# Kernel optimization log

Hardware: AMD Instinct MI355X
Metric: run time of the kernel (lower is better)

The kernel has to match this reference:

```python
import jax, jax.numpy as jnp
import numpy as np

N = 50000      # nodes
E = 800000     # edges (before self loops)
F_IN = 512     # input feature dim (num_features)
D = 128        # hidden_dim
NBLK = 3       # num_layers - 1
EPS = 1e-5


def _layernorm(x, g, b):
    mu = x.mean(-1, keepdims=True)
    var = ((x - mu) ** 2).mean(-1, keepdims=True)
    return (x - mu) / jnp.sqrt(var + EPS) * g + b


def _gatv2(x, Wl, bl, Wr, br, att, bias, src, dst, n):
    # PyG GATv2Conv, heads=1, eval mode (attention dropout off), self loops in src/dst
    xl = x @ Wl + bl                      # [N, D] messages (x_j side)
    xr = x @ Wr + br                      # [N, D] target side (x_i)
    e = jax.nn.leaky_relu(xl[src] + xr[dst], negative_slope=0.2)  # [E', D]
    score = e @ att                       # [E']
    smax = jax.ops.segment_max(score, dst, num_segments=n)
    ex = jnp.exp(score - smax[dst])
    denom = jax.ops.segment_sum(ex, dst, num_segments=n)
    alpha = ex / denom[dst]               # segment softmax over incoming edges
    out = jax.ops.segment_sum(alpha[:, None] * xl[src], dst, num_segments=n)
    return out + bias


def setup_inputs() -> dict:
    key = jax.random.key(0)
    ks = jax.random.split(key, 32)
    w = lambda k, shape: (jax.random.normal(k, shape, jnp.float32) * 0.02)
    p = {}
    p["x"] = jax.random.normal(ks[0], (N, F_IN), jnp.float32)
    p["edge_index"] = jax.random.randint(ks[1], (2, E), 0, N)
    p["emb_W"] = w(ks[2], (F_IN, D)); p["emb_b"] = jnp.zeros((D,), jnp.float32)
    p["ln1_g"] = jnp.ones((NBLK, D), jnp.float32); p["ln1_b"] = jnp.zeros((NBLK, D), jnp.float32)
    p["gat_Wl"] = w(ks[3], (NBLK, D, D)); p["gat_bl"] = jnp.zeros((NBLK, D), jnp.float32)
    p["gat_Wr"] = w(ks[4], (NBLK, D, D)); p["gat_br"] = jnp.zeros((NBLK, D), jnp.float32)
    p["gat_att"] = w(ks[5], (NBLK, D)); p["gat_bias"] = jnp.zeros((NBLK, D), jnp.float32)
    for i in range(NBLK):
        h = D * (i + 1)  # mlp_ratio = level = i+1
        p[f"mlp_w1_{i}"] = w(ks[6 + 2 * i], (D, h))
        p[f"mlp_w2_{i}"] = w(ks[7 + 2 * i], (h, D))
    p["attn_Wa"] = w(ks[12], (D, D)); p["attn_ba"] = jnp.zeros((D,), jnp.float32)
    p["attn_Wb"] = w(ks[13], (D, D)); p["attn_bb"] = jnp.zeros((D,), jnp.float32)
    p["attn_Wc"] = w(ks[14], (D, 1)); p["attn_bc"] = jnp.zeros((1,), jnp.float32)
    p["rho_W"] = w(ks[15], (D, D)); p["rho_b"] = jnp.zeros((D,), jnp.float32)
    p["cls_W"] = w(ks[16], (D, 4)); p["cls_b"] = jnp.zeros((4,), jnp.float32)
    return p


def reference(x, edge_index, emb_W, emb_b, ln1_g, ln1_b, gat_Wl, gat_bl, gat_Wr, gat_br,
              gat_att, gat_bias, mlp_w1_0, mlp_w2_0, mlp_w1_1, mlp_w2_1, mlp_w1_2, mlp_w2_2,
              attn_Wa, attn_ba, attn_Wb, attn_bb, attn_Wc, attn_bc, rho_W, rho_b, cls_W, cls_b):
    n = x.shape[0]
    sl = jnp.arange(n, dtype=edge_index.dtype)
    src = jnp.concatenate([edge_index[0], sl])  # add self loops (GATv2Conv default)
    dst = jnp.concatenate([edge_index[1], sl])
    h = jax.nn.relu(x @ emb_W + emb_b)          # embedding (dropout off)
    mlps = [(mlp_w1_0, mlp_w2_0), (mlp_w1_1, mlp_w2_1), (mlp_w1_2, mlp_w2_2)]
    for i in range(NBLK):
        hn = _layernorm(h, ln1_g[i], ln1_b[i])
        h = h + _gatv2(hn, gat_Wl[i], gat_bl[i], gat_Wr[i], gat_br[i], gat_att[i], gat_bias[i], src, dst, n)
        w1, w2 = mlps[i]
        # NOTE: original forward applies channel_mix directly on x (norm2 is unused)
        h = h + jax.nn.gelu(h @ w1, approximate=False) @ w2
    # Attn_Net_Gated pooling
    a = jnp.tanh(h @ attn_Wa + attn_ba)
    b = jax.nn.sigmoid(h @ attn_Wb + attn_bb)
    A = ((a * b) @ attn_Wc + attn_bc).T          # [1, N]
    h_path = jax.nn.softmax(A, axis=1) @ h       # [1, D]
    hr = jax.nn.relu(h_path @ rho_W + rho_b)
    logits = hr @ cls_W + cls_b                  # [1, 4]
    Y_hat = jnp.argmax(logits, axis=1, keepdims=True)
    hazards = jax.nn.sigmoid(logits)
    S = jnp.cumprod(1.0 - hazards, axis=1)
    return (hazards, S, Y_hat, logits)
```

## Files before the change

### kernel.cpp

```cpp
#include <hip/hip_runtime.h>
#include <math.h>


#define D 128
#define NBLK 3
#define STG_STRIDE 132
#define S16 136
#define ROWS 128
#define BT 512

typedef __attribute__((ext_vector_type(8))) short bf16x8;
typedef __attribute__((ext_vector_type(4))) float f32x4;

static __device__ __forceinline__ float bf2f(unsigned short u) {
    union { unsigned i; float f; } c; c.i = ((unsigned)u) << 16; return c.f;
}
static __device__ __forceinline__ unsigned short f2bf(float f) {
    union { float f; unsigned i; } c; c.f = f;
    unsigned r = c.i + 0x7fff + ((c.i >> 16) & 1);
    return (unsigned short)(r >> 16);
}
static __device__ __forceinline__ void gl16(const unsigned short* g, unsigned short* l) {
    __builtin_amdgcn_global_load_lds((const __attribute__((address_space(1))) void*)g,
                                     (__attribute__((address_space(3))) void*)l, 16, 0, 0);
}
static __device__ __forceinline__ float gelu_f(float x) {
    return 0.5f * x * (1.f + erff(x * 0.70710678118654752f));
}

__global__ void zero_k(int* deg, int* fill, float* red, int n) {
    int i = blockIdx.x * blockDim.x + threadIdx.x;
    if (i < n) { deg[i] = 0; fill[i] = 0; }
    if (i < 132) red[i] = 0.f;
}

__global__ void hist_k(const int* __restrict__ dst, int* __restrict__ deg, int E) {
    int e = blockIdx.x * blockDim.x + threadIdx.x;
    if (e < E) atomicAdd(&deg[dst[e]], 1);
}

__global__ __launch_bounds__(256) void blockscan_k(const int* __restrict__ deg,
                                                   int* __restrict__ rowptr,
                                                   int* __restrict__ bsum, int n) {
    __shared__ int tmp[256];
    const int tid = threadIdx.x;
    const int i = blockIdx.x * 256 + tid;
    int v = (i < n) ? deg[i] : 0;
    tmp[tid] = v;
    __syncthreads();
#pragma unroll
    for (int off = 1; off < 256; off <<= 1) {
        int t = (tid >= off) ? tmp[tid - off] : 0;
        __syncthreads();
        tmp[tid] += t;
        __syncthreads();
    }
    if (i < n) rowptr[i + 1] = tmp[tid];
    if (tid == 255) bsum[blockIdx.x] = tmp[255];
}

__global__ __launch_bounds__(256) void scansums_k(int* __restrict__ bsum, int nb) {
    __shared__ int tmp[256];
    const int tid = threadIdx.x;
    int v = (tid < nb) ? bsum[tid] : 0;
    tmp[tid] = v;
    __syncthreads();
#pragma unroll
    for (int off = 1; off < 256; off <<= 1) {
        int t = (tid >= off) ? tmp[tid - off] : 0;
        __syncthreads();
        tmp[tid] += t;
        __syncthreads();
    }
    if (tid < nb) bsum[tid] = tmp[tid];
}

__global__ __launch_bounds__(256) void addoff_k(int* __restrict__ rowptr,
                                                const int* __restrict__ bsum, int n) {
    int i = blockIdx.x * 256 + threadIdx.x;
    if (i == 0) rowptr[0] = 0;
    if (i < n && blockIdx.x > 0) rowptr[i + 1] += bsum[blockIdx.x - 1];
}

__global__ void scatter_k(const int* __restrict__ src, const int* __restrict__ dst,
                          const int* __restrict__ rowptr, int* __restrict__ fill,
                          int* __restrict__ esrc, int E) {
    int e = blockIdx.x * blockDim.x + threadIdx.x;
    if (e < E) {
        int d = dst[e];
        int pos = rowptr[d] + atomicAdd(&fill[d], 1);
        esrc[pos] = src[e];
    }
}

struct WDesc { const float* s; unsigned short* d; int K; int M; };
struct WPack { WDesc w[21]; };

__global__ __launch_bounds__(256) void wprep_k(WPack p) {
    WDesc d = p.w[blockIdx.y];
    const int nc = d.K / 32;
    const int chunks = (d.M / 16) * nc * 64;
    for (int i = blockIdx.x * 256 + threadIdx.x; i < chunks; i += gridDim.x * 256) {
        const int l = i & 63;
        const int c = (i >> 6) % nc;
        const int t = i / (64 * nc);
        const int m = t * 16 + (l & 15);
        const int kb = c * 32 + ((l >> 4) & 3) * 8;
#pragma unroll
        for (int j = 0; j < 8; ++j)
            d.d[(size_t)i * 8 + j] = f2bf(d.s[(size_t)(kb + j) * d.M + m]);
    }
}

__global__ __launch_bounds__(256) void bcat_k(const float* bl, const float* br,
                                              const float* ba, const float* bb,
                                              float* sb) {
    const int t = threadIdx.x;
    for (int i = 0; i < 3; ++i)
        sb[i * 256 + t] = (t < 128) ? bl[i * 128 + t] : br[i * 128 + t - 128];
    sb[3 * 256 + t] = (t < 128) ? ba[t] : bb[t - 128];
}


static __device__ __forceinline__ void stage_blob(const unsigned short* src,
                                                  unsigned short* wls, int tid) {
#pragma unroll
    for (int i = 0; i < 4; ++i) {
        const int idx = i * BT + tid;
        gl16(src + (size_t)idx * 8, &wls[idx * 8]);
    }
}

static __device__ __forceinline__ void pf_issue(const unsigned short* src, int tid,
                                                float4 pf[4]) {
#pragma unroll
    for (int i = 0; i < 4; ++i)
        pf[i] = *(const float4*)(src + (size_t)(i * BT + tid) * 8);
}
static __device__ __forceinline__ void pf_commit(unsigned short* wls, int tid,
                                                 const float4 pf[4]) {
#pragma unroll
    for (int i = 0; i < 4; ++i)
        *(float4*)(&wls[(i * BT + tid) * 8]) = pf[i];
}

static __device__ __forceinline__ void mfma32(const bf16x8 a[4],
                                              const unsigned short* wls,
                                              int l, f32x4 acc[8]) {
#pragma unroll
    for (int c = 0; c < 4; ++c)
#pragma unroll
        for (int t = 0; t < 8; ++t) {
            const bf16x8 bfr = *(const bf16x8*)&wls[((t * 4 + c) * 64 + l) * 8];
            acc[t] = __builtin_amdgcn_mfma_f32_16x16x32_bf16(a[c], bfr, acc[t], 0, 0, 0);
        }
}

static __device__ __forceinline__ void ln_row(float av[4][8], const float* lng,
                                              const float* lnb, int q) {
    float s = 0.f;
#pragma unroll
    for (int c = 0; c < 4; ++c)
#pragma unroll
        for (int j = 0; j < 8; ++j) s += av[c][j];
    s += __shfl_xor(s, 16, 64); s += __shfl_xor(s, 32, 64);
    const float mu = s * (1.f / 128.f);
    float vv = 0.f;
#pragma unroll
    for (int c = 0; c < 4; ++c)
#pragma unroll
        for (int j = 0; j < 8; ++j) { const float dd = av[c][j] - mu; vv += dd * dd; }
    vv += __shfl_xor(vv, 16, 64); vv += __shfl_xor(vv, 32, 64);
    const float rs = rsqrtf(vv * (1.f / 128.f) + 1e-5f);
#pragma unroll
    for (int c = 0; c < 4; ++c) {
        const int kb = c * 32 + q * 8;
        const float4 g0 = *(const float4*)(lng + kb);
        const float4 g1 = *(const float4*)(lng + kb + 4);
        const float4 b0 = *(const float4*)(lnb + kb);
        const float4 b1 = *(const float4*)(lnb + kb + 4);
        const float gg[8] = {g0.x, g0.y, g0.z, g0.w, g1.x, g1.y, g1.z, g1.w};
        const float bb[8] = {b0.x, b0.y, b0.z, b0.w, b1.x, b1.y, b1.z, b1.w};
#pragma unroll
        for (int j = 0; j < 8; ++j)
            av[c][j] = (av[c][j] - mu) * rs * gg[j] + bb[j];
    }
}

static __device__ __forceinline__ void xwrite(const f32x4 acc[8], const float* sb256,
                                              unsigned short* X, int rnd, int rowbase,
                                              int w, int q, int l15, int N) {
#pragma unroll
    for (int t = 0; t < 8; ++t) {
        const int col = rnd * 128 + t * 16 + l15;
        const float bv = sb256[col];
#pragma unroll
        for (int rr = 0; rr < 4; ++rr) {
            const int row = rowbase + w * 16 + q * 4 + rr;
            if (row < N) X[(size_t)row * 256 + col] = f2bf(acc[t][rr] + bv);
        }
    }
}

__global__ __launch_bounds__(BT) void start_k(const float* __restrict__ x,
                                              const unsigned short* __restrict__ embc,
                                              const float* __restrict__ emb_b,
                                              const unsigned short* __restrict__ gatc,
                                              const float* __restrict__ lng,
                                              const float* __restrict__ lnb,
                                              const float* __restrict__ sb256,
                                              float* __restrict__ H,
                                              unsigned short* __restrict__ X, int N) {
    __shared__ __align__(16) char smem[ROWS * STG_STRIDE * 4];
    unsigned short* wls = (unsigned short*)smem;
    float* stg = (float*)smem;
    const int tid = threadIdx.x;
    const int w = tid >> 6, l = tid & 63, q = l >> 4, l15 = l & 15;
    const int rowbase = blockIdx.x * ROWS;
    int r = rowbase + w * 16 + l15;
    const bool rv = r < N; if (!rv) r = N - 1;
    float4 pf[4];

    f32x4 accH[8];
#pragma unroll
    for (int t = 0; t < 8; ++t) accH[t] = (f32x4){0.f, 0.f, 0.f, 0.f};

    stage_blob(embc, wls, tid);
    __syncthreads();

#pragma unroll
    for (int rnd = 0; rnd < 4; ++rnd) {
        const unsigned short* nb = (rnd < 3) ? embc + (size_t)(rnd + 1) * 16384 : gatc;
        pf_issue(nb, tid, pf);
        bf16x8 afr[4];
#pragma unroll
        for (int c = 0; c < 4; ++c) {
            const float* ap = x + (size_t)r * 512 + rnd * 128 + c * 32 + q * 8;
            const float4 v0 = *(const float4*)ap;
            const float4 v1 = *(const float4*)(ap + 4);
            afr[c][0] = (short)f2bf(v0.x); afr[c][1] = (short)f2bf(v0.y);
            afr[c][2] = (short)f2bf(v0.z); afr[c][3] = (short)f2bf(v0.w);
            afr[c][4] = (short)f2bf(v1.x); afr[c][5] = (short)f2bf(v1.y);
            afr[c][6] = (short)f2bf(v1.z); afr[c][7] = (short)f2bf(v1.w);
        }
        mfma32(afr, wls, l, accH);
        __syncthreads();
        if (rnd < 3) { pf_commit(wls, tid, pf); __syncthreads(); }
    }

#pragma unroll
    for (int t = 0; t < 8; ++t) {
        const int col = t * 16 + l15;
        const float bv = emb_b[col];
#pragma unroll
        for (int rr = 0; rr < 4; ++rr) {
            const int row = rowbase + w * 16 + q * 4 + rr;
            const float hv = fmaxf(accH[t][rr] + bv, 0.f);
            if (row < N) H[(size_t)row * D + col] = hv;
            stg[(w * 16 + q * 4 + rr) * STG_STRIDE + col] = hv;
        }
    }
    float av[4][8];
#pragma unroll
    for (int c = 0; c < 4; ++c)
#pragma unroll
        for (int j = 0; j < 8; ++j)
            av[c][j] = stg[(w * 16 + l15) * STG_STRIDE + c * 32 + q * 8 + j];
    ln_row(av, lng, lnb, q);
    bf16x8 xfr[4];
#pragma unroll
    for (int c = 0; c < 4; ++c)
#pragma unroll
        for (int j = 0; j < 8; ++j) xfr[c][j] = (short)f2bf(av[c][j]);

    __syncthreads();
    pf_commit(wls, tid, pf);
    __syncthreads();

    pf_issue(gatc + 16384, tid, pf);
    f32x4 acc[8];
#pragma unroll
    for (int t = 0; t < 8; ++t) acc[t] = (f32x4){0.f, 0.f, 0.f, 0.f};
    mfma32(xfr, wls, l, acc);
    xwrite(acc, sb256, X, 0, rowbase, w, q, l15, N);
    __syncthreads();
    pf_commit(wls, tid, pf);
    __syncthreads();

#pragma unroll
    for (int t = 0; t < 8; ++t) acc[t] = (f32x4){0.f, 0.f, 0.f, 0.f};
    mfma32(xfr, wls, l, acc);
    xwrite(acc, sb256, X, 1, rowbase, w, q, l15, N);
}

template <int NMR>
__global__ __launch_bounds__(BT) void bridge_k(float* __restrict__ H,
                                               const unsigned short* __restrict__ w1c,
                                               const unsigned short* __restrict__ w2c,
                                               const unsigned short* __restrict__ gatc,
                                               const float* __restrict__ lng,
                                               const float* __restrict__ lnb,
                                               const float* __restrict__ sb256,
                                               unsigned short* __restrict__ X, int N) {
    __shared__ __align__(16) char smem[ROWS * STG_STRIDE * 4];
    unsigned short* wls   = (unsigned short*)smem;
    unsigned short* stg16 = (unsigned short*)(smem + 32768);
    float*          stgF  = (float*)smem;
    const int tid = threadIdx.x;
    const int w = tid >> 6, l = tid & 63, q = l >> 4, l15 = l & 15;
    const int rowbase = blockIdx.x * ROWS;
    int r = rowbase + w * 16 + l15;
    const bool rv = r < N; if (!rv) r = N - 1;
    float4 pf[4];

    stage_blob(w1c, wls, tid);

    float av[4][8];
    bf16x8 afr[4];
#pragma unroll
    for (int c = 0; c < 4; ++c) {
        const float* ap = H + (size_t)r * D + c * 32 + q * 8;
        const float4 v0 = *(const float4*)ap;
        const float4 v1 = *(const float4*)(ap + 4);
        av[c][0] = v0.x; av[c][1] = v0.y; av[c][2] = v0.z; av[c][3] = v0.w;
        av[c][4] = v1.x; av[c][5] = v1.y; av[c][6] = v1.z; av[c][7] = v1.w;
#pragma unroll
        for (int j = 0; j < 8; ++j) afr[c][j] = (short)f2bf(av[c][j]);
    }

    f32x4 accH[8];
#pragma unroll
    for (int t = 0; t < 8; ++t) accH[t] = (f32x4){0.f, 0.f, 0.f, 0.f};
    __syncthreads();

#pragma unroll
    for (int rnd = 0; rnd < NMR; ++rnd) {
        pf_issue(w2c + (size_t)rnd * 16384, tid, pf);
        f32x4 accT[8];
#pragma unroll
        for (int t = 0; t < 8; ++t) accT[t] = (f32x4){0.f, 0.f, 0.f, 0.f};
        mfma32(afr, wls, l, accT);
#pragma unroll
        for (int t = 0; t < 8; ++t)
#pragma unroll
            for (int rr = 0; rr < 4; ++rr)
                stg16[(w * 16 + q * 4 + rr) * S16 + t * 16 + l15] = f2bf(gelu_f(accT[t][rr]));
        __syncthreads();
        pf_commit(wls, tid, pf);
        __syncthreads();
        const unsigned short* nb = (rnd + 1 < NMR) ? w1c + (size_t)(rnd + 1) * 16384 : gatc;
        pf_issue(nb, tid, pf);
        bf16x8 tfr[4];
#pragma unroll
        for (int c = 0; c < 4; ++c)
            tfr[c] = *(const bf16x8*)&stg16[(w * 16 + l15) * S16 + c * 32 + q * 8];
        mfma32(tfr, wls, l, accH);
        __syncthreads();
        if (rnd + 1 < NMR) { pf_commit(wls, tid, pf); __syncthreads(); }
    }

#pragma unroll
    for (int t = 0; t < 8; ++t)
#pragma unroll
        for (int rr = 0; rr < 4; ++rr)
            stgF[(w * 16 + q * 4 + rr) * STG_STRIDE + t * 16 + l15] = accH[t][rr];
#pragma unroll
    for (int c = 0; c < 4; ++c)
#pragma unroll
        for (int j = 0; j < 8; ++j)
            av[c][j] += stgF[(w * 16 + l15) * STG_STRIDE + c * 32 + q * 8 + j];

    if (rv) {
#pragma unroll
        for (int c = 0; c < 4; ++c) {
            float* hp = H + (size_t)r * D + c * 32 + q * 8;
            *(float4*)hp       = make_float4(av[c][0], av[c][1], av[c][2], av[c][3]);
            *(float4*)(hp + 4) = make_float4(av[c][4], av[c][5], av[c][6], av[c][7]);
        }
    }

    ln_row(av, lng, lnb, q);
    bf16x8 xfr[4];
#pragma unroll
    for (int c = 0; c < 4; ++c)
#pragma unroll
        for (int j = 0; j < 8; ++j) xfr[c][j] = (short)f2bf(av[c][j]);

    __syncthreads();
    pf_commit(wls, tid, pf);
    __syncthreads();

    pf_issue(gatc + 16384, tid, pf);
    f32x4 acc[8];
#pragma unroll
    for (int t = 0; t < 8; ++t) acc[t] = (f32x4){0.f, 0.f, 0.f, 0.f};
    mfma32(xfr, wls, l, acc);
    xwrite(acc, sb256, X, 0, rowbase, w, q, l15, N);
    __syncthreads();
    pf_commit(wls, tid, pf);
    __syncthreads();

#pragma unroll
    for (int t = 0; t < 8; ++t) acc[t] = (f32x4){0.f, 0.f, 0.f, 0.f};
    mfma32(xfr, wls, l, acc);
    xwrite(acc, sb256, X, 1, rowbase, w, q, l15, N);
}

__global__ __launch_bounds__(BT) void head_k(const float* __restrict__ H,
                                             const unsigned short* __restrict__ w1c,
                                             const unsigned short* __restrict__ w2c,
                                             const unsigned short* __restrict__ attc,
                                             const float* __restrict__ sb256,
                                             const float* __restrict__ Wc,
                                             const float* __restrict__ bc,
                                             float* __restrict__ red, int N) {
    __shared__ __align__(16) char smem[ROWS * STG_STRIDE * 4];
    unsigned short* wls   = (unsigned short*)smem;
    unsigned short* stg16 = (unsigned short*)(smem + 32768);
    float*          stgF  = (float*)smem;
    __shared__ float sacc[8][128];
    __shared__ float sdn[8];
    const int tid = threadIdx.x;
    const int w = tid >> 6, l = tid & 63, q = l >> 4, l15 = l & 15;
    const int rowbase = blockIdx.x * ROWS;
    int r = rowbase + w * 16 + l15;
    if (r > N - 1) r = N - 1;
    float4 pf[4];

    stage_blob(w1c, wls, tid);

    float av[4][8];
    bf16x8 afr[4];
#pragma unroll
    for (int c = 0; c < 4; ++c) {
        const float* ap = H + (size_t)r * D + c * 32 + q * 8;
        const float4 v0 = *(const float4*)ap;
        const float4 v1 = *(const float4*)(ap + 4);
        av[c][0] = v0.x; av[c][1] = v0.y; av[c][2] = v0.z; av[c][3] = v0.w;
        av[c][4] = v1.x; av[c][5] = v1.y; av[c][6] = v1.z; av[c][7] = v1.w;
#pragma unroll
        for (int j = 0; j < 8; ++j) afr[c][j] = (short)f2bf(av[c][j]);
    }

    f32x4 accH[8];
#pragma unroll
    for (int t = 0; t < 8; ++t) accH[t] = (f32x4){0.f, 0.f, 0.f, 0.f};
    __syncthreads();

#pragma unroll
    for (int rnd = 0; rnd < 3; ++rnd) {
        pf_issue(w2c + (size_t)rnd * 16384, tid, pf);
        f32x4 accT[8];
#pragma unroll
        for (int t = 0; t < 8; ++t) accT[t] = (f32x4){0.f, 0.f, 0.f, 0.f};
        mfma32(afr, wls, l, accT);
#pragma unroll
        for (int t = 0; t < 8; ++t)
#pragma unroll
            for (int rr = 0; rr < 4; ++rr)
                stg16[(w * 16 + q * 4 + rr) * S16 + t * 16 + l15] = f2bf(gelu_f(accT[t][rr]));
        __syncthreads();
        pf_commit(wls, tid, pf);
        __syncthreads();
        const unsigned short* nb = (rnd + 1 < 3) ? w1c + (size_t)(rnd + 1) * 16384 : attc;
        pf_issue(nb, tid, pf);
        bf16x8 tfr[4];
#pragma unroll
        for (int c = 0; c < 4; ++c)
            tfr[c] = *(const bf16x8*)&stg16[(w * 16 + l15) * S16 + c * 32 + q * 8];
        mfma32(tfr, wls, l, accH);
        __syncthreads();
        if (rnd + 1 < 3) { pf_commit(wls, tid, pf); __syncthreads(); }
    }

#pragma unroll
    for (int t = 0; t < 8; ++t)
#pragma unroll
        for (int rr = 0; rr < 4; ++rr)
            stgF[(w * 16 + q * 4 + rr) * STG_STRIDE + t * 16 + l15] = accH[t][rr];
#pragma unroll
    for (int c = 0; c < 4; ++c)
#pragma unroll
        for (int j = 0; j < 8; ++j)
            av[c][j] += stgF[(w * 16 + l15) * STG_STRIDE + c * 32 + q * 8 + j];
#pragma unroll
    for (int c = 0; c < 4; ++c)
#pragma unroll
        for (int j = 0; j < 8; ++j) afr[c][j] = (short)f2bf(av[c][j]);

    __syncthreads();
    pf_commit(wls, tid, pf);
    __syncthreads();

    pf_issue(attc + 16384, tid, pf);
    float th[8][4];
    f32x4 acc[8];
#pragma unroll
    for (int t = 0; t < 8; ++t) acc[t] = (f32x4){0.f, 0.f, 0.f, 0.f};
    mfma32(afr, wls, l, acc);
#pragma unroll
    for (int t = 0; t < 8; ++t) {
        const float bv = sb256[t * 16 + l15];
#pragma unroll
        for (int rr = 0; rr < 4; ++rr) th[t][rr] = tanhf(acc[t][rr] + bv);
    }
    __syncthreads();
    pf_commit(wls, tid, pf);
    __syncthreads();

#pragma unroll
    for (int t = 0; t < 8; ++t) acc[t] = (f32x4){0.f, 0.f, 0.f, 0.f};
    mfma32(afr, wls, l, acc);

    float pa[4] = {0.f, 0.f, 0.f, 0.f};
#pragma unroll
    for (int t = 0; t < 8; ++t) {
        const float bv = sb256[128 + t * 16 + l15];
        const float wcv = Wc[t * 16 + l15];
#pragma unroll
        for (int rr = 0; rr < 4; ++rr) {
            const float sg = 1.f / (1.f + __expf(-(acc[t][rr] + bv)));
            pa[rr] = fmaf(th[t][rr] * sg, wcv, pa[rr]);
        }
    }
#pragma unroll
    for (int m = 1; m < 16; m <<= 1)
#pragma unroll
        for (int rr = 0; rr < 4; ++rr) pa[rr] += __shfl_xor(pa[rr], m, 64);

    const float bcv = bc[0];
    float wgt[4];
#pragma unroll
    for (int rr = 0; rr < 4; ++rr) {
        const int row = rowbase + w * 16 + q * 4 + rr;
        wgt[rr] = (row < N) ? __expf(pa[rr] + bcv) : 0.f;
    }
    float s = wgt[0] + wgt[1] + wgt[2] + wgt[3];
    s += __shfl_xor(s, 16, 64);
    s += __shfl_xor(s, 32, 64);
    if (l == 0) sdn[w] = s;

    const int sl = ((l15 >> 2) << 4);
    float wv[4];
#pragma unroll
    for (int rr = 0; rr < 4; ++rr) wv[rr] = __shfl(wgt[rr], sl, 64);
    const int rsel = l15 & 3;
    const float wm = (rsel == 0) ? wv[0] : (rsel == 1) ? wv[1] : (rsel == 2) ? wv[2] : wv[3];

#pragma unroll
    for (int c = 0; c < 4; ++c) {
        float pv[8];
#pragma unroll
        for (int j = 0; j < 8; ++j) pv[j] = wm * av[c][j];
#pragma unroll
        for (int m = 1; m < 16; m <<= 1)
#pragma unroll
            for (int j = 0; j < 8; ++j) pv[j] += __shfl_xor(pv[j], m, 64);
        if (l15 == 0) {
#pragma unroll
            for (int j = 0; j < 8; ++j) sacc[w][c * 32 + q * 8 + j] = pv[j];
        }
    }
    __syncthreads();
    if (tid < 128) {
        float tot = 0.f;
#pragma unroll
        for (int ww = 0; ww < 8; ++ww) tot += sacc[ww][tid];
        atomicAdd(&red[tid], tot);
    }
    if (tid == 0) {
        float ds = 0.f;
#pragma unroll
        for (int ww = 0; ww < 8; ++ww) ds += sdn[ww];
        atomicAdd(&red[128], ds);
    }
}

__global__ __launch_bounds__(256) void gat3_k(const unsigned short* __restrict__ X,
                                              const float* __restrict__ att,
                                              const float* __restrict__ gbias,
                                              const int* __restrict__ rowptr,
                                              const int* __restrict__ esrc,
                                              float* __restrict__ H, int n) {
    const int l = threadIdx.x & 63;
    const int node = blockIdx.x * 4 + (threadIdx.x >> 6);
    if (node >= n) return;
    const int q = l >> 4;
    const int d0 = (l & 15) * 8;

    float a8[8], xr[8], xs[8];
    {
        const float4 t0 = *(const float4*)&att[d0];
        const float4 t1 = *(const float4*)&att[d0 + 4];
        a8[0] = t0.x; a8[1] = t0.y; a8[2] = t0.z; a8[3] = t0.w;
        a8[4] = t1.x; a8[5] = t1.y; a8[6] = t1.z; a8[7] = t1.w;
        const bf16x8 uxs = *(const bf16x8*)&X[(size_t)node * 256 + d0];
        const bf16x8 uxr = *(const bf16x8*)&X[(size_t)node * 256 + 128 + d0];
#pragma unroll
        for (int j = 0; j < 8; ++j) {
            xs[j] = bf2f((unsigned short)uxs[j]);
            xr[j] = bf2f((unsigned short)uxr[j]);
        }
    }

    float sc = 0.f;
#pragma unroll
    for (int j = 0; j < 8; ++j) {
        const float e = xs[j] + xr[j];
        sc = fmaf(a8[j], fmaxf(e, 0.2f * e), sc);
    }
#pragma unroll
    for (int m = 1; m < 16; m <<= 1) sc += __shfl_xor(sc, m, 64);
    const float wself = __expf(sc);
    float dsum = (q == 0) ? wself : 0.f;
    float acc[8];
#pragma unroll
    for (int j = 0; j < 8; ++j) acc[j] = (q == 0) ? wself * xs[j] : 0.f;

    const int p1 = rowptr[node + 1];
    int p = rowptr[node] + q;
    bool v0 = p < p1, v1 = p + 4 < p1, v2 = p + 8 < p1;
    int i2 = v2 ? esrc[p + 8] : 0;
    bf16x8 u0, u1;
    if (v0) u0 = *(const bf16x8*)&X[(size_t)esrc[p] * 256 + d0];
    if (v1) u1 = *(const bf16x8*)&X[(size_t)esrc[p + 4] * 256 + d0];
    while (v0) {
        bf16x8 u2;
        if (v2) u2 = *(const bf16x8*)&X[(size_t)i2 * 256 + d0];
        const bool v3 = p + 12 < p1;
        const int i3 = v3 ? esrc[p + 12] : 0;

        float xl[8];
#pragma unroll
        for (int j = 0; j < 8; ++j) xl[j] = bf2f((unsigned short)u0[j]);
        float e_sc = 0.f;
#pragma unroll
        for (int j = 0; j < 8; ++j) {
            const float e = xl[j] + xr[j];
            e_sc = fmaf(a8[j], fmaxf(e, 0.2f * e), e_sc);
        }
#pragma unroll
        for (int m = 1; m < 16; m <<= 1) e_sc += __shfl_xor(e_sc, m, 64);
        const float wgt = __expf(e_sc);
        dsum += wgt;
#pragma unroll
        for (int j = 0; j < 8; ++j) acc[j] = fmaf(wgt, xl[j], acc[j]);

        u0 = u1; u1 = u2; i2 = i3;
        v0 = v1; v1 = v2; v2 = v3;
        p += 4;
    }

#pragma unroll
    for (int m = 16; m < 64; m <<= 1) {
        dsum += __shfl_xor(dsum, m, 64);
#pragma unroll
        for (int j = 0; j < 8; ++j) acc[j] += __shfl_xor(acc[j], m, 64);
    }

    if (q == 0) {
        const float inv = 1.f / dsum;
        const size_t o = (size_t)node * D + d0;
        float4 h0 = *(const float4*)&H[o];
        float4 h1 = *(const float4*)&H[o + 4];
        float hv[8] = {h0.x, h0.y, h0.z, h0.w, h1.x, h1.y, h1.z, h1.w};
#pragma unroll
        for (int j = 0; j < 8; ++j) hv[j] += acc[j] * inv + gbias[d0 + j];
        *(float4*)&H[o]     = make_float4(hv[0], hv[1], hv[2], hv[3]);
        *(float4*)&H[o + 4] = make_float4(hv[4], hv[5], hv[6], hv[7]);
    }
}

__global__ __launch_bounds__(128) void final_k(const float* __restrict__ red,
                                               const float* __restrict__ rho_W,
                                               const float* __restrict__ rho_b,
                                               const float* __restrict__ cls_W,
                                               const float* __restrict__ cls_b,
                                               float* __restrict__ out) {
    __shared__ float hp[128];
    __shared__ float hr[128];
    __shared__ float lg[4];
    const int t = threadIdx.x;
    hp[t] = red[t] / red[128];
    __syncthreads();
    float s = rho_b[t];
    for (int k = 0; k < 128; ++k) s = fmaf(hp[k], rho_W[k * 128 + t], s);
    hr[t] = fmaxf(s, 0.f);
    __syncthreads();
    if (t < 4) {
        float l = cls_b[t];
        for (int k = 0; k < 128; ++k) l = fmaf(hr[k], cls_W[k * 4 + t], l);
        lg[t] = l;
    }
    __syncthreads();
    if (t == 0) {
        float hz[4], S[4];
        for (int c = 0; c < 4; ++c) hz[c] = 1.f / (1.f + expf(-lg[c]));
        S[0] = 1.f - hz[0];
        for (int c = 1; c < 4; ++c) S[c] = S[c - 1] * (1.f - hz[c]);
        int am = 0; float bm = lg[0];
        for (int c = 1; c < 4; ++c) if (lg[c] > bm) { bm = lg[c]; am = c; }
        out[0] = hz[0]; out[1] = hz[1]; out[2] = hz[2]; out[3] = hz[3];
        out[4] = S[0];  out[5] = S[1];  out[6] = S[2];  out[7] = S[3];
        out[8] = (float)am;
        out[9] = lg[0]; out[10] = lg[1]; out[11] = lg[2]; out[12] = lg[3];
    }
}

static inline int cdiv(int a, int b) { return (a + b - 1) / b; }

extern "C" void kernel_launch(void* const* d_in, const int* in_sizes, int n_in,
                              void* d_out, int out_size, void* d_ws, size_t ws_size,
                              hipStream_t stream) {
    const float* x      = (const float*)d_in[0];
    const int*   ei     = (const int*)d_in[1];
    const float* emb_W  = (const float*)d_in[2];
    const float* emb_b  = (const float*)d_in[3];
    const float* ln1_g  = (const float*)d_in[4];
    const float* ln1_b  = (const float*)d_in[5];
    const float* gat_Wl = (const float*)d_in[6];
    const float* gat_bl = (const float*)d_in[7];
    const float* gat_Wr = (const float*)d_in[8];
    const float* gat_br = (const float*)d_in[9];
    const float* gat_att  = (const float*)d_in[10];
    const float* gat_bias = (const float*)d_in[11];
    const float* mlp_w1[NBLK] = {(const float*)d_in[12], (const float*)d_in[14], (const float*)d_in[16]};
    const float* mlp_w2[NBLK] = {(const float*)d_in[13], (const float*)d_in[15], (const float*)d_in[17]};
    const float* attn_Wa = (const float*)d_in[18];
    const float* attn_ba = (const float*)d_in[19];
    const float* attn_Wb = (const float*)d_in[20];
    const float* attn_bb = (const float*)d_in[21];
    const float* attn_Wc = (const float*)d_in[22];
    const float* attn_bc = (const float*)d_in[23];
    const float* rho_W   = (const float*)d_in[24];
    const float* rho_b   = (const float*)d_in[25];
    const float* cls_W   = (const float*)d_in[26];
    const float* cls_b   = (const float*)d_in[27];
    float* out = (float*)d_out;

    const int N = in_sizes[0] / 512;
    const int E = in_sizes[1] / 2;
    const int* src = ei;
    const int* dst = ei + E;
    const int gx = cdiv(N, ROWS);

    char* base = (char*)d_ws;
    float* H = (float*)base;
    unsigned short* X = (unsigned short*)(H + (size_t)N * D);
    float* red  = (float*)(X + (size_t)N * 256);
    float* sb   = red + 132;
    unsigned short* wbuf = (unsigned short*)(sb + 1024);
    int* esrc   = (int*)(wbuf + 393216);
    int* deg    = esrc + E;
    int* rowptr = deg + N;
    int* fill   = rowptr + N + 1;
    int* bsum   = fill + N;

    unsigned short* embT = wbuf;
    unsigned short* gatT = wbuf + 4 * 16384;
    unsigned short* w1T0 = gatT + 6 * 16384;
    unsigned short* w1T1 = w1T0 + 16384;
    unsigned short* w1T2 = w1T1 + 2 * 16384;
    unsigned short* w2T0 = w1T2 + 3 * 16384;
    unsigned short* w2T1 = w2T0 + 16384;
    unsigned short* w2T2 = w2T1 + 2 * 16384;
    unsigned short* attT = w2T2 + 3 * 16384;
    unsigned short* w1T[NBLK] = {w1T0, w1T1, w1T2};
    unsigned short* w2T[NBLK] = {w2T0, w2T1, w2T2};

    const int nb = cdiv(N, 256);
    zero_k<<<cdiv(N, 256), 256, 0, stream>>>(deg, fill, red, N);
    hist_k<<<cdiv(E, 256), 256, 0, stream>>>(dst, deg, E);
    blockscan_k<<<nb, 256, 0, stream>>>(deg, rowptr, bsum, N);
    scansums_k<<<1, 256, 0, stream>>>(bsum, nb);
    addoff_k<<<nb, 256, 0, stream>>>(rowptr, bsum, N);
    scatter_k<<<cdiv(E, 256), 256, 0, stream>>>(src, dst, rowptr, fill, esrc, E);

    {
        WPack p;
        int di = 0;
        for (int r = 0; r < 4; ++r)
            p.w[di++] = {emb_W + (size_t)r * 128 * 128, embT + (size_t)r * 16384, 128, 128};
        for (int i = 0; i < 3; ++i) {
            p.w[di++] = {gat_Wl + (size_t)i * 16384, gatT + (size_t)(2 * i) * 16384, 128, 128};
            p.w[di++] = {gat_Wr + (size_t)i * 16384, gatT + (size_t)(2 * i + 1) * 16384, 128, 128};
        }
        for (int i = 0; i < 3; ++i)
            p.w[di++] = {mlp_w1[i], w1T[i], 128, 128 * (i + 1)};
        for (int i = 0; i < 3; ++i)
            for (int r = 0; r <= i; ++r)
                p.w[di++] = {mlp_w2[i] + (size_t)r * 128 * 128, w2T[i] + (size_t)r * 16384, 128, 128};
        p.w[di++] = {attn_Wa, attT, 128, 128};
        p.w[di++] = {attn_Wb, attT + 16384, 128, 128};
        wprep_k<<<dim3(32, 21), 256, 0, stream>>>(p);
    }
    bcat_k<<<1, 256, 0, stream>>>(gat_bl, gat_br, attn_ba, attn_bb, sb);

    start_k<<<gx, BT, 0, stream>>>(x, embT, emb_b, gatT, ln1_g, ln1_b, sb, H, X, N);
    gat3_k<<<cdiv(N, 4), 256, 0, stream>>>(X, gat_att, gat_bias, rowptr, esrc, H, N);

    bridge_k<1><<<gx, BT, 0, stream>>>(H, w1T[0], w2T[0], gatT + 2 * 16384,
                                       ln1_g + D, ln1_b + D, sb + 256, X, N);
    gat3_k<<<cdiv(N, 4), 256, 0, stream>>>(X, gat_att + D, gat_bias + D, rowptr, esrc, H, N);

    bridge_k<2><<<gx, BT, 0, stream>>>(H, w1T[1], w2T[1], gatT + 4 * 16384,
                                       ln1_g + 2 * D, ln1_b + 2 * D, sb + 512, X, N);
    gat3_k<<<cdiv(N, 4), 256, 0, stream>>>(X, gat_att + 2 * D, gat_bias + 2 * D, rowptr, esrc, H, N);

    head_k<<<gx, BT, 0, stream>>>(H, w1T[2], w2T[2], attT, sb + 3 * 256,
                                  attn_Wc, attn_bc, red, N);
    final_k<<<1, 128, 0, stream>>>(red, rho_W, rho_b, cls_W, cls_b, out);
}
```

Measured before the change: 713.5 us.

## Double-buffer weight blobs in LDS via direct global-to-LDS loads

Replaces the register prefetch plus LDS commit scheme with two LDS weight buffers filled directly by global_load_lds, so the next weight chunk streams into the idle buffer while MFMA runs on the current one. This removes register staging and roughly one barrier per round. The GELU intermediate now reuses the first weight buffer with an XOR swizzle to avoid bank conflicts, in place of a separate padded stage. The risk is that correctness depends on the async LDS loads completing before the barriers, and the extra buffer changes LDS aliasing with the float staging area.

```diff
diff --git a/kernel.cpp b/kernel.cpp
--- a/kernel.cpp
+++ b/kernel.cpp
@@ -5,7 +5,6 @@
 #define D 128
 #define NBLK 3
 #define STG_STRIDE 132
-#define S16 136
 #define ROWS 128
 #define BT 512
 
@@ -26,6 +25,9 @@
 }
 static __device__ __forceinline__ float gelu_f(float x) {
     return 0.5f * x * (1.f + erff(x * 0.70710678118654752f));
+}
+static __device__ __forceinline__ int gswz(int row, int col) {
+    return row * 128 + (col ^ ((row & 7) << 3));
 }
 
 __global__ void zero_k(int* deg, int* fill, float* red, int n) {
@@ -131,19 +133,6 @@
     }
 }
 
-static __device__ __forceinline__ void pf_issue(const unsigned short* src, int tid,
-                                                float4 pf[4]) {
-#pragma unroll
-    for (int i = 0; i < 4; ++i)
-        pf[i] = *(const float4*)(src + (size_t)(i * BT + tid) * 8);
-}
-static __device__ __forceinline__ void pf_commit(unsigned short* wls, int tid,
-                                                 const float4 pf[4]) {
-#pragma unroll
-    for (int i = 0; i < 4; ++i)
-        *(float4*)(&wls[(i * BT + tid) * 8]) = pf[i];
-}
-
 static __device__ __forceinline__ void mfma32(const bf16x8 a[4],
                                               const unsigned short* wls,
                                               int l, f32x4 acc[8]) {
@@ -212,26 +201,27 @@
                                               float* __restrict__ H,
                                               unsigned short* __restrict__ X, int N) {
     __shared__ __align__(16) char smem[ROWS * STG_STRIDE * 4];
-    unsigned short* wls = (unsigned short*)smem;
+    unsigned short* bufA = (unsigned short*)smem;
+    unsigned short* bufB = bufA + 16384;
     float* stg = (float*)smem;
     const int tid = threadIdx.x;
     const int w = tid >> 6, l = tid & 63, q = l >> 4, l15 = l & 15;
     const int rowbase = blockIdx.x * ROWS;
     int r = rowbase + w * 16 + l15;
     const bool rv = r < N; if (!rv) r = N - 1;
-    float4 pf[4];
 
     f32x4 accH[8];
 #pragma unroll
     for (int t = 0; t < 8; ++t) accH[t] = (f32x4){0.f, 0.f, 0.f, 0.f};
 
-    stage_blob(embc, wls, tid);
+    stage_blob(embc, bufA, tid);
     __syncthreads();
 
 #pragma unroll
     for (int rnd = 0; rnd < 4; ++rnd) {
-        const unsigned short* nb = (rnd < 3) ? embc + (size_t)(rnd + 1) * 16384 : gatc;
-        pf_issue(nb, tid, pf);
+        unsigned short* cur = (rnd & 1) ? bufB : bufA;
+        unsigned short* nxt = (rnd & 1) ? bufA : bufB;
+        if (rnd < 3) stage_blob(embc + (size_t)(rnd + 1) * 16384, nxt, tid);
         bf16x8 afr[4];
 #pragma unroll
         for (int c = 0; c < 4; ++c) {
@@ -243,9 +233,8 @@
             afr[c][4] = (short)f2bf(v1.x); afr[c][5] = (short)f2bf(v1.y);
             afr[c][6] = (short)f2bf(v1.z); afr[c][7] = (short)f2bf(v1.w);
         }
-        mfma32(afr, wls, l, accH);
-        __syncthreads();
-        if (rnd < 3) { pf_commit(wls, tid, pf); __syncthreads(); }
+        mfma32(afr, cur, l, accH);
+        __syncthreads();
     }
 
 #pragma unroll
@@ -274,22 +263,20 @@
         for (int j = 0; j < 8; ++j) xfr[c][j] = (short)f2bf(av[c][j]);
 
     __syncthreads();
-    pf_commit(wls, tid, pf);
-    __syncthreads();
-
-    pf_issue(gatc + 16384, tid, pf);
+    stage_blob(gatc, bufA, tid);
+    __syncthreads();
+
+    stage_blob(gatc + 16384, bufB, tid);
     f32x4 acc[8];
 #pragma unroll
     for (int t = 0; t < 8; ++t) acc[t] = (f32x4){0.f, 0.f, 0.f, 0.f};
-    mfma32(xfr, wls, l, acc);
+    mfma32(xfr, bufA, l, acc);
     xwrite(acc, sb256, X, 0, rowbase, w, q, l15, N);
     __syncthreads();
-    pf_commit(wls, tid, pf);
-    __syncthreads();
 
 #pragma unroll
     for (int t = 0; t < 8; ++t) acc[t] = (f32x4){0.f, 0.f, 0.f, 0.f};
-    mfma32(xfr, wls, l, acc);
+    mfma32(xfr, bufB, l, acc);
     xwrite(acc, sb256, X, 1, rowbase, w, q, l15, N);
 }
 
@@ -303,17 +290,16 @@
                                                const float* __restrict__ sb256,
                                                unsigned short* __restrict__ X, int N) {
     __shared__ __align__(16) char smem[ROWS * STG_STRIDE * 4];
-    unsigned short* wls   = (unsigned short*)smem;
-    unsigned short* stg16 = (unsigned short*)(smem + 32768);
-    float*          stgF  = (float*)smem;
+    unsigned short* bufA = (unsigned short*)smem;
+    unsigned short* bufB = bufA + 16384;
+    float* stgF = (float*)smem;
     const int tid = threadIdx.x;
     const int w = tid >> 6, l = tid & 63, q = l >> 4, l15 = l & 15;
     const int rowbase = blockIdx.x * ROWS;
     int r = rowbase + w * 16 + l15;
     const bool rv = r < N; if (!rv) r = N - 1;
-    float4 pf[4];
-
-    stage_blob(w1c, wls, tid);
+
+    stage_blob(w1c, bufA, tid);
 
     float av[4][8];
     bf16x8 afr[4];
@@ -335,28 +321,26 @@
 
 #pragma unroll
     for (int rnd = 0; rnd < NMR; ++rnd) {
-        pf_issue(w2c + (size_t)rnd * 16384, tid, pf);
+        stage_blob(w2c + (size_t)rnd * 16384, bufB, tid);
         f32x4 accT[8];
 #pragma unroll
         for (int t = 0; t < 8; ++t) accT[t] = (f32x4){0.f, 0.f, 0.f, 0.f};
-        mfma32(afr, wls, l, accT);
+        mfma32(afr, bufA, l, accT);
+        __syncthreads();
 #pragma unroll
         for (int t = 0; t < 8; ++t)
 #pragma unroll
             for (int rr = 0; rr < 4; ++rr)
-                stg16[(w * 16 + q * 4 + rr) * S16 + t * 16 + l15] = f2bf(gelu_f(accT[t][rr]));
-        __syncthreads();
-        pf_commit(wls, tid, pf);
-        __syncthreads();
-        const unsigned short* nb = (rnd + 1 < NMR) ? w1c + (size_t)(rnd + 1) * 16384 : gatc;
-        pf_issue(nb, tid, pf);
+                bufA[gswz(w * 16 + q * 4 + rr, t * 16 + l15)] = f2bf(gelu_f(accT[t][rr]));
         bf16x8 tfr[4];
 #pragma unroll
         for (int c = 0; c < 4; ++c)
-            tfr[c] = *(const bf16x8*)&stg16[(w * 16 + l15) * S16 + c * 32 + q * 8];
-        mfma32(tfr, wls, l, accH);
-        __syncthreads();
-        if (rnd + 1 < NMR) { pf_commit(wls, tid, pf); __syncthreads(); }
+            tfr[c] = *(const bf16x8*)&bufA[gswz(w * 16 + l15, c * 32 + q * 8)];
+        __syncthreads();
+        if (rnd + 1 < NMR)
+            stage_blob(w1c + (size_t)(rnd + 1) * 16384, bufA, tid);
+        mfma32(tfr, bufB, l, accH);
+        __syncthreads();
     }
 
 #pragma unroll
@@ -387,22 +371,20 @@
         for (int j = 0; j < 8; ++j) xfr[c][j] = (short)f2bf(av[c][j]);
 
     __syncthreads();
-    pf_commit(wls, tid, pf);
-    __syncthreads();
-
-    pf_issue(gatc + 16384, tid, pf);
+    stage_blob(gatc, bufA, tid);
+    __syncthreads();
+
+    stage_blob(gatc + 16384, bufB, tid);
     f32x4 acc[8];
 #pragma unroll
     for (int t = 0; t < 8; ++t) acc[t] = (f32x4){0.f, 0.f, 0.f, 0.f};
-    mfma32(xfr, wls, l, acc);
+    mfma32(xfr, bufA, l, acc);
     xwrite(acc, sb256, X, 0, rowbase, w, q, l15, N);
     __syncthreads();
-    pf_commit(wls, tid, pf);
-    __syncthreads();
 
 #pragma unroll
     for (int t = 0; t < 8; ++t) acc[t] = (f32x4){0.f, 0.f, 0.f, 0.f};
-    mfma32(xfr, wls, l, acc);
+    mfma32(xfr, bufB, l, acc);
     xwrite(acc, sb256, X, 1, rowbase, w, q, l15, N);
 }
 
@@ -415,9 +397,9 @@
                                              const float* __restrict__ bc,
                                              float* __restrict__ red, int N) {
     __shared__ __align__(16) char smem[ROWS * STG_STRIDE * 4];
-    unsigned short* wls   = (unsigned short*)smem;
-    unsigned short* stg16 = (unsigned short*)(smem + 32768);
-    float*          stgF  = (float*)smem;
+    unsigned short* bufA = (unsigned short*)smem;
+    unsigned short* bufB = bufA + 16384;
+    float* stgF = (float*)smem;
     __shared__ float sacc[8][128];
     __shared__ float sdn[8];
     const int tid = threadIdx.x;
@@ -425,9 +407,8 @@
     const int rowbase = blockIdx.x * ROWS;
     int r = rowbase + w * 16 + l15;
     if (r > N - 1) r = N - 1;
-    float4 pf[4];
-
-    stage_blob(w1c, wls, tid);
+
+    stage_blob(w1c, bufA, tid);
 
     float av[4][8];
     bf16x8 afr[4];
@@ -449,28 +430,26 @@
 
 #pragma unroll
     for (int rnd = 0; rnd < 3; ++rnd) {
-        pf_issue(w2c + (size_t)rnd * 16384, tid, pf);
+        stage_blob(w2c + (size_t)rnd * 16384, bufB, tid);
         f32x4 accT[8];
 #pragma unroll
         for (int t = 0; t < 8; ++t) accT[t] = (f32x4){0.f, 0.f, 0.f, 0.f};
-        mfma32(afr, wls, l, accT);
+        mfma32(afr, bufA, l, accT);
+        __syncthreads();
 #pragma unroll
         for (int t = 0; t < 8; ++t)
 #pragma unroll
             for (int rr = 0; rr < 4; ++rr)
-                stg16[(w * 16 + q * 4 + rr) * S16 + t * 16 + l15] = f2bf(gelu_f(accT[t][rr]));
-        __syncthreads();
-        pf_commit(wls, tid, pf);
-        __syncthreads();
-        const unsigned short* nb = (rnd + 1 < 3) ? w1c + (size_t)(rnd + 1) * 16384 : attc;
-        pf_issue(nb, tid, pf);
+                bufA[gswz(w * 16 + q * 4 + rr, t * 16 + l15)] = f2bf(gelu_f(accT[t][rr]));
         bf16x8 tfr[4];
 #pragma unroll
         for (int c = 0; c < 4; ++c)
-            tfr[c] = *(const bf16x8*)&stg16[(w * 16 + l15) * S16 + c * 32 + q * 8];
-        mfma32(tfr, wls, l, accH);
-        __syncthreads();
-        if (rnd + 1 < 3) { pf_commit(wls, tid, pf); __syncthreads(); }
+            tfr[c] = *(const bf16x8*)&bufA[gswz(w * 16 + l15, c * 32 + q * 8)];
+        __syncthreads();
+        if (rnd + 1 < 3)
+            stage_blob(w1c + (size_t)(rnd + 1) * 16384, bufA, tid);
+        mfma32(tfr, bufB, l, accH);
+        __syncthreads();
     }
 
 #pragma unroll
@@ -489,15 +468,15 @@
         for (int j = 0; j < 8; ++j) afr[c][j] = (short)f2bf(av[c][j]);
 
     __syncthreads();
-    pf_commit(wls, tid, pf);
-    __syncthreads();
-
-    pf_issue(attc + 16384, tid, pf);
+    stage_blob(attc, bufA, tid);
+    __syncthreads();
+
+    stage_blob(attc + 16384, bufB, tid);
     float th[8][4];
     f32x4 acc[8];
 #pragma unroll
     for (int t = 0; t < 8; ++t) acc[t] = (f32x4){0.f, 0.f, 0.f, 0.f};
-    mfma32(afr, wls, l, acc);
+    mfma32(afr, bufA, l, acc);
 #pragma unroll
     for (int t = 0; t < 8; ++t) {
         const float bv = sb256[t * 16 + l15];
@@ -505,12 +484,10 @@
         for (int rr = 0; rr < 4; ++rr) th[t][rr] = tanhf(acc[t][rr] + bv);
     }
     __syncthreads();
-    pf_commit(wls, tid, pf);
-    __syncthreads();
 
 #pragma unroll
     for (int t = 0; t < 8; ++t) acc[t] = (f32x4){0.f, 0.f, 0.f, 0.f};
-    mfma32(afr, wls, l, acc);
+    mfma32(afr, bufB, l, acc);
 
     float pa[4] = {0.f, 0.f, 0.f, 0.f};
 #pragma unroll
```

Measured after the change: 636.7 us (median of 2 runs). -10.8%, faster.
